# Kernel tuning notes

Measured on AMD Instinct MI355X. Metric: run time of the kernel, lower is better.

## Reference

```python
import jax, jax.numpy as jnp
import numpy as np

THRESH = 0.1          # affinity threshold from init_kwargs
SCALES = (1, 2, 4, 8, 16)  # dyadic diffusion scales 2^0..2^4


def compute_dist(X):
    # X: [N, d] -> squared-euclidean pairwise distances via Gram matrix
    G = X @ X.T
    dg = jnp.diag(G)
    return dg[None, :] + dg[:, None] - 2.0 * G


def _diffuse(P, F):
    # returns [P^1 F, P^2 F, P^4 F, P^8 F, P^16 F] via 16 sequential applies
    outs = []
    cur = F
    for step in range(1, SCALES[-1] + 1):
        cur = P @ cur
        if step in SCALES:
            outs.append(cur)
    return outs


def _wavelet_bank(P, F):
    # lazy diffusion wavelets: psi_0 = I - P, psi_j = P^{2^{j-1}} - P^{2^j}
    lows = [F] + _diffuse(P, F)            # t = 0,1,2,4,8,16
    psis = [lows[j] - lows[j + 1] for j in range(len(lows) - 1)]  # 5 wavelets
    return psis, lows[-1]                  # (wavelet coeffs, low-pass P^16 F)


def _gwt_features(X):
    # X: [N, d] reweighted point cloud -> [N, 16*d] scattering features
    N, d = X.shape
    W = jnp.exp(-compute_dist(X) / 10.0)
    W = jnp.where(W < THRESH, jnp.zeros_like(W), W)   # sparsify affinity
    deg = W.sum(axis=1, keepdims=True)                # self-loop w=1 => deg>=1
    P = 0.5 * (jnp.eye(N, dtype=X.dtype) + W / deg)   # lazy random walk
    psis, low = _wavelet_bank(P, X)
    firsts = [jnp.abs(p) for p in psis]
    U = jnp.concatenate(firsts, axis=1)               # [N, 5*d] diffuse all at once
    psis2, _ = _wavelet_bank(P, U)
    # second order: |psi_{j2} |psi_{j1} x|| only for j2 > j1 (10 pairs)
    seconds = [jnp.abs(psis2[j2][:, : j2 * d]) for j2 in range(1, len(psis2))]
    return jnp.concatenate([low] + firsts + seconds, axis=1)  # [N, (1+5+10)*d]


def setup_inputs() -> dict:
    key = jax.random.key(0)
    k1, k2 = jax.random.split(key)
    point_clouds = jax.random.normal(k1, (4, 2048, 3), dtype=jnp.float32)
    alphas = jax.random.uniform(k2, (4, 3), dtype=jnp.float32)  # learned param
    return {"point_clouds": point_clouds, "alphas": alphas}


def reference(point_clouds, alphas):
    # point_clouds: [B, N, d]; alphas: [K, d]
    Xb = point_clouds[:, None, :, :] * alphas[None, :, None, :]  # [B, K, N, d]
    feats = jax.vmap(jax.vmap(_gwt_features))(Xb)                # [B, K, N, 16d]
    # per-cloud: cat over K along feature dim then mean over nodes == mean then flatten
    return feats.mean(axis=2).reshape(feats.shape[0], -1)        # [B, K*16*d]
```

## Files before the change

### kernel.cpp

```cpp
#include <hip/hip_runtime.h>
#include <hip/hip_bf16.h>


#define NN 2048
#define NPAIR 16

typedef _Float16 half8 __attribute__((ext_vector_type(8)));
typedef _Float16 f16x2 __attribute__((ext_vector_type(2)));
typedef float f32x4 __attribute__((ext_vector_type(4)));

extern "C" __device__ f16x2 __ocml_exp2_2f16(f16x2);

#define C2F 0.28853900817779268f
#define CWF -0.14426950408889634f
#define NL2T 3.3219280948873623f

__global__ __launch_bounds__(256) void initpack_k(const float* __restrict__ pc,
                                                  const float* __restrict__ alphas,
                                                  float* __restrict__ Xs,
                                                  _Float16* __restrict__ XT,
                                                  _Float16* __restrict__ Xp) {
    int gid = blockIdx.x * 256 + threadIdx.x;
    if (gid >= NPAIR * NN) return;
    int p = gid >> 11, i = gid & (NN - 1);
    int b = p >> 2, k = p & 3;
    const float* pcr = pc + ((size_t)b * NN + i) * 3;
    const float* al  = alphas + k * 3;
    float x = pcr[0] * al[0], y = pcr[1] * al[1], z = pcr[2] * al[2];
    float q = CWF * (x * x + y * y + z * z);
    float4 o; o.x = x; o.y = y; o.z = z; o.w = q;
    ((float4*)Xs)[gid] = o;
    _Float16* xt = XT + (size_t)p * 16 * NN + i;
    xt[0 * NN] = (_Float16)x;
    xt[1 * NN] = (_Float16)y;
    xt[2 * NN] = (_Float16)z;
    xt[3 * NN] = (_Float16)1.0f;
#pragma unroll
    for (int n = 4; n < 16; ++n) xt[n * NN] = (_Float16)0.f;
    _Float16* xp = Xp + ((size_t)p * 1024 + (i >> 1)) * 8 + (i & 1);
    xp[0] = (_Float16)x; xp[2] = (_Float16)y;
    xp[4] = (_Float16)z; xp[6] = (_Float16)q;
}

template<bool FIRST, bool DUAL, bool BUILDU>
__global__ __launch_bounds__(512, DUAL ? 4 : 8)
void apply_k(const float* __restrict__ Xs, const _Float16* __restrict__ Xp,
             float* __restrict__ ihd,
             const _Float16* __restrict__ cur1, _Float16* __restrict__ out1,
             float* __restrict__ lvl1, int t1,
             const _Float16* __restrict__ cur2, _Float16* __restrict__ out2,
             float* __restrict__ lvl2, int t2,
             const float* __restrict__ LT1u, _Float16* __restrict__ UTp) {
    constexpr int SMSZ = DUAL ? 8192 : 4352;
    __shared__ __align__(16) float smem[SMSZ];
    const int tid  = threadIdx.x;
    const int lane = tid & 63;
    const int wv   = tid >> 6;
    const int p    = blockIdx.y;
    const int m0   = blockIdx.x * 32;
    const int idx16 = lane & 15, quad = lane >> 4;

    {
        const float4* src = (const float4*)(Xp + (size_t)p * 8192);
        float4* dst = (float4*)smem;
        dst[tid]       = src[tid];
        dst[tid + 512] = src[tid + 512];
    }
    __syncthreads();

    f16x2 qi2[2], xx2[2], xy2[2], xz2[2];
#pragma unroll
    for (int s = 0; s < 2; ++s) {
        float4 v = *(const float4*)(Xs + ((size_t)p * NN + m0 + s * 16 + idx16) * 4);
        _Float16 q = (_Float16)(v.w + NL2T);
        _Float16 x = (_Float16)(C2F * v.x);
        _Float16 y = (_Float16)(C2F * v.y);
        _Float16 z = (_Float16)(C2F * v.z);
        qi2[s] = (f16x2){q, q}; xx2[s] = (f16x2){x, x};
        xy2[s] = (f16x2){y, y}; xz2[s] = (f16x2){z, z};
    }
    const f16x2 SC2 = (f16x2){(_Float16)32768.f, (_Float16)32768.f};

    const _Float16* bp1 = cur1 + ((size_t)p * 16 + idx16) * NN + wv * 256 + quad * 8;
    const _Float16* bp2 = DUAL ? cur2 + ((size_t)p * 16 + idx16) * NN + wv * 256 + quad * 8
                               : nullptr;
    f32x4 acc1[2] = {{0.f,0.f,0.f,0.f},{0.f,0.f,0.f,0.f}};
    f32x4 acc2[2] = {{0.f,0.f,0.f,0.f},{0.f,0.f,0.f,0.f}};

    for (int kc = 0; kc < 8; ++kc) {
        const int pb = wv * 128 + kc * 16 + quad * 4;
        half8 bf1 = *(const half8*)(bp1 + kc * 32);
        half8 bf2;
        if (DUAL) bf2 = *(const half8*)(bp2 + kc * 32);
        union { f16x2 h2[4]; half8 h8; } af[2];
#pragma unroll
        for (int jp = 0; jp < 4; ++jp) {
            union { float4 f; f16x2 h[4]; } e;
            e.f = ((const float4*)smem)[pb + jp];
#pragma unroll
            for (int s = 0; s < 2; ++s) {
                f16x2 tv = qi2[s] + e.h[3];
                tv = __builtin_elementwise_fma(xx2[s], e.h[0], tv);
                tv = __builtin_elementwise_fma(xy2[s], e.h[1], tv);
                tv = __builtin_elementwise_fma(xz2[s], e.h[2], tv);
                f16x2 u = __builtin_elementwise_min(tv, tv * SC2);
                af[s].h2[jp] = __ocml_exp2_2f16(u);
            }
        }
#pragma unroll
        for (int s = 0; s < 2; ++s) {
            acc1[s] = __builtin_amdgcn_mfma_f32_16x16x32_f16(af[s].h8, bf1, acc1[s], 0, 0, 0);
            if (DUAL)
                acc2[s] = __builtin_amdgcn_mfma_f32_16x16x32_f16(af[s].h8, bf2, acc2[s], 0, 0, 0);
        }
    }

    const int n = tid & 15, rloc = tid >> 4;
    const int s2 = rloc >> 4, mloc = rloc & 15;
    const int base = s2 * 256 + (mloc >> 2) * 64 + (mloc & 3);
    const int row = m0 + rloc;
    float ihEff;
    if (!FIRST) ihEff = 0.1f * ihd[p * NN + row];

    __syncthreads();
#pragma unroll
    for (int s = 0; s < 2; ++s)
        *(f32x4*)&smem[wv * 512 + s * 256 + lane * 4] = acc1[s];
    if (DUAL) {
#pragma unroll
        for (int s = 0; s < 2; ++s)
            *(f32x4*)&smem[4096 + wv * 512 + s * 256 + lane * 4] = acc2[s];
    }
    __syncthreads();

    float o1v;
    {
        float sum = 0.f;
#pragma unroll
        for (int g = 0; g < 8; ++g) sum += smem[g * 512 + base + n * 4];
        if (FIRST) {
            float deg10 = 0.f;
#pragma unroll
            for (int g = 0; g < 8; ++g) deg10 += smem[g * 512 + base + 12];
            float ih = 5.0f / deg10;
            if (n == 3) ihd[p * NN + row] = ih;
            ihEff = 0.1f * ih;
        }
        float cv = (float)cur1[((size_t)p * 16 + n) * NN + row];
        o1v = 0.5f * cv + ihEff * sum;
        out1[((size_t)p * 16 + n) * NN + row] = (_Float16)o1v;
        if (lvl1) lvl1[(((size_t)p * 5 + t1) * 16 + n) * NN + row] = o1v;
    }
    if (DUAL) {
        float sum = 0.f;
#pragma unroll
        for (int g = 0; g < 8; ++g) sum += smem[4096 + g * 512 + base + n * 4];
        float cv = (float)cur2[((size_t)p * 16 + n) * NN + row];
        float o = 0.5f * cv + ihEff * sum;
        out2[((size_t)p * 16 + n) * NN + row] = (_Float16)o;
        if (lvl2) lvl2[(((size_t)p * 5 + t2) * 16 + n) * NN + row] = o;
    }
    if (BUILDU) {
        if (n < 3) smem[4096 + n * 32 + rloc] = o1v;
        __syncthreads();
        _Float16 uv = (_Float16)0.f;
        if (n < 12) {
            const int jw = n / 3, c = n - 3 * jw;
            float a = (jw == 0) ? Xs[((size_t)p * NN + row) * 4 + c]
                                : LT1u[(((size_t)p * 5 + (jw - 1)) * 16 + c) * NN + row];
            float bb = (jw == 3) ? smem[4096 + c * 32 + rloc]
                                 : LT1u[(((size_t)p * 5 + jw) * 16 + c) * NN + row];
            uv = (_Float16)fabsf(a - bb);
        }
        UTp[((size_t)p * 16 + n) * NN + row] = uv;
    }
}

__global__ __launch_bounds__(64) void reduce_k(const float* __restrict__ Xs,
                                               const float* __restrict__ LT1,
                                               const float* __restrict__ LT2,
                                               float* __restrict__ out) {
    int f = blockIdx.x, p = blockIdx.y, lane = threadIdx.x;
    const float* l1 = LT1 + (size_t)p * 5 * 16 * NN;
    const float* l2 = LT2 + (size_t)p * 5 * 16 * NN;
    float s = 0.f;
    for (int m = lane; m < NN; m += 64) {
        float v;
        if (f < 3) {
            v = l1[((size_t)4 * 16 + f) * NN + m];
        } else if (f < 18) {
            int j = (f - 3) / 3, c = (f - 3) % 3;
            float a = (j == 0) ? Xs[((size_t)p * NN + m) * 4 + c]
                               : l1[((size_t)(j - 1) * 16 + c) * NN + m];
            float b = l1[((size_t)j * 16 + c) * NN + m];
            v = fabsf(a - b);
        } else {
            int gg = f - 18, j2, uc;
            if (gg < 3)       { j2 = 1; uc = gg; }
            else if (gg < 9)  { j2 = 2; uc = gg - 3; }
            else if (gg < 18) { j2 = 3; uc = gg - 9; }
            else              { j2 = 4; uc = gg - 18; }
            v = fabsf(l2[((size_t)(j2 - 1) * 16 + uc) * NN + m]
                    - l2[((size_t)j2 * 16 + uc) * NN + m]);
        }
        s += v;
    }
#pragma unroll
    for (int off = 32; off > 0; off >>= 1) s += __shfl_down(s, off, 64);
    if (lane == 0) out[p * 48 + f] = s * (1.0f / NN);
}

extern "C" void kernel_launch(void* const* d_in, const int* in_sizes, int n_in,
                              void* d_out, int out_size, void* d_ws, size_t ws_size,
                              hipStream_t stream) {
    const float* pc     = (const float*)d_in[0];
    const float* alphas = (const float*)d_in[1];
    float* outp = (float*)d_out;

    char* base = (char*)d_ws;
    size_t off = 0;
    auto carve = [&](size_t bytes) -> void* {
        void* r = base + off;
        off = (off + bytes + 255) & ~(size_t)255;
        return r;
    };
    float*     Xs  = (float*)carve((size_t)NPAIR * NN * 4 * sizeof(float));
    _Float16*  Xp  = (_Float16*)carve((size_t)NPAIR * 1024 * 8 * 2);
    float*     ihd = (float*)carve((size_t)NPAIR * NN * sizeof(float));
    _Float16*  XT  = (_Float16*)carve((size_t)NPAIR * 16 * NN * 2);
    _Float16*  UT  = (_Float16*)carve((size_t)NPAIR * 16 * NN * 2);
    _Float16*  pA  = (_Float16*)carve((size_t)NPAIR * 16 * NN * 2);
    _Float16*  pB  = (_Float16*)carve((size_t)NPAIR * 16 * NN * 2);
    _Float16*  pC  = (_Float16*)carve((size_t)NPAIR * 16 * NN * 2);
    _Float16*  pD  = (_Float16*)carve((size_t)NPAIR * 16 * NN * 2);
    float*     LT1 = (float*)carve((size_t)NPAIR * 5 * 16 * NN * sizeof(float));
    float*     LT2 = (float*)carve((size_t)NPAIR * 5 * 16 * NN * sizeof(float));

    dim3 gridA(NN / 32, NPAIR);

    initpack_k<<<dim3((NPAIR * NN) / 256), 256, 0, stream>>>(pc, alphas, Xs, XT, Xp);

    const _Float16* c1 = XT;
    int slot = 0;
    for (int step = 1; step <= 8; ++step) {
        _Float16* o1 = (c1 == pA) ? pB : pA;
        bool sv = (step & (step - 1)) == 0;
        float* lv = sv ? LT1 : nullptr;
        if (step == 1)
            apply_k<true, false, false><<<gridA, 512, 0, stream>>>(Xs, Xp, ihd,
                c1, o1, lv, slot, nullptr, nullptr, nullptr, 0, nullptr, nullptr);
        else if (step == 8)
            apply_k<false, false, true><<<gridA, 512, 0, stream>>>(Xs, Xp, ihd,
                c1, o1, lv, slot, nullptr, nullptr, nullptr, 0, LT1, UT);
        else
            apply_k<false, false, false><<<gridA, 512, 0, stream>>>(Xs, Xp, ihd,
                c1, o1, lv, slot, nullptr, nullptr, nullptr, 0, nullptr, nullptr);
        if (sv) ++slot;
        c1 = o1;
    }

    const _Float16* c2 = UT;
    int slot2 = 0;
    for (int i = 1; i <= 8; ++i) {
        _Float16* o1 = (c1 == pA) ? pB : pA;
        _Float16* o2 = (c2 == pC) ? pD : pC;
        float* lv1 = (i == 8) ? LT1 : nullptr;
        bool sv2 = (i & (i - 1)) == 0;
        float* lv2 = sv2 ? LT2 : nullptr;
        apply_k<false, true, false><<<gridA, 512, 0, stream>>>(Xs, Xp, ihd,
            c1, o1, lv1, 4, c2, o2, lv2, slot2, nullptr, nullptr);
        if (sv2) ++slot2;
        c1 = o1; c2 = o2;
    }

    for (int i = 9; i <= 16; ++i) {
        _Float16* o2 = (c2 == pC) ? pD : pC;
        float* lv2 = (i == 16) ? LT2 : nullptr;
        apply_k<false, false, false><<<gridA, 512, 0, stream>>>(Xs, Xp, ihd,
            c2, o2, lv2, 4, nullptr, nullptr, nullptr, 0, nullptr, nullptr);
        c2 = o2;
    }

    reduce_k<<<dim3(48, NPAIR), 64, 0, stream>>>(Xs, LT1, LT2, outp);
}
```

Before: 484.1 us.

## Pack first-order chain and U signals into one 16-column diffusion stream

Before, steps 9-16 of the first-order diffusion and steps 1-8 of the second-order diffusion ran as two separate 16-column right-hand sides in a dual-MFMA kernel. Now, at step 8, the x-chain (columns 0-3) and the 12 |psi| columns share one 16-column buffer, so a single-RHS kernel is used for all 16 later steps. The dual kernel and its extra buffers are removed, and the reduction reads P^16 x from the second level table. The launch count stays the same, but each later launch does half the MFMA and B-operand traffic, and the dual kernel's lower occupancy bound goes away.

```diff
diff --git a/kernel.cpp b/kernel.cpp
--- a/kernel.cpp
+++ b/kernel.cpp
@@ -42,17 +42,14 @@
     xp[4] = (_Float16)z; xp[6] = (_Float16)q;
 }
 
-template<bool FIRST, bool DUAL, bool BUILDU>
-__global__ __launch_bounds__(512, DUAL ? 4 : 8)
+template<bool FIRST, bool BUILDU>
+__global__ __launch_bounds__(512, 8)
 void apply_k(const float* __restrict__ Xs, const _Float16* __restrict__ Xp,
              float* __restrict__ ihd,
-             const _Float16* __restrict__ cur1, _Float16* __restrict__ out1,
-             float* __restrict__ lvl1, int t1,
-             const _Float16* __restrict__ cur2, _Float16* __restrict__ out2,
-             float* __restrict__ lvl2, int t2,
-             const float* __restrict__ LT1u, _Float16* __restrict__ UTp) {
-    constexpr int SMSZ = DUAL ? 8192 : 4352;
-    __shared__ __align__(16) float smem[SMSZ];
+             const _Float16* __restrict__ cur, _Float16* __restrict__ out,
+             float* __restrict__ lvl, int t,
+             const float* __restrict__ LT1u) {
+    __shared__ __align__(16) float smem[4352];
     const int tid  = threadIdx.x;
     const int lane = tid & 63;
     const int wv   = tid >> 6;
@@ -81,17 +78,12 @@
     }
     const f16x2 SC2 = (f16x2){(_Float16)32768.f, (_Float16)32768.f};
 
-    const _Float16* bp1 = cur1 + ((size_t)p * 16 + idx16) * NN + wv * 256 + quad * 8;
-    const _Float16* bp2 = DUAL ? cur2 + ((size_t)p * 16 + idx16) * NN + wv * 256 + quad * 8
-                               : nullptr;
-    f32x4 acc1[2] = {{0.f,0.f,0.f,0.f},{0.f,0.f,0.f,0.f}};
-    f32x4 acc2[2] = {{0.f,0.f,0.f,0.f},{0.f,0.f,0.f,0.f}};
+    const _Float16* bp = cur + ((size_t)p * 16 + idx16) * NN + wv * 256 + quad * 8;
+    f32x4 acc[2] = {{0.f,0.f,0.f,0.f},{0.f,0.f,0.f,0.f}};
 
     for (int kc = 0; kc < 8; ++kc) {
         const int pb = wv * 128 + kc * 16 + quad * 4;
-        half8 bf1 = *(const half8*)(bp1 + kc * 32);
-        half8 bf2;
-        if (DUAL) bf2 = *(const half8*)(bp2 + kc * 32);
+        half8 bf = *(const half8*)(bp + kc * 32);
         union { f16x2 h2[4]; half8 h8; } af[2];
 #pragma unroll
         for (int jp = 0; jp < 4; ++jp) {
@@ -108,71 +100,54 @@
             }
         }
 #pragma unroll
-        for (int s = 0; s < 2; ++s) {
-            acc1[s] = __builtin_amdgcn_mfma_f32_16x16x32_f16(af[s].h8, bf1, acc1[s], 0, 0, 0);
-            if (DUAL)
-                acc2[s] = __builtin_amdgcn_mfma_f32_16x16x32_f16(af[s].h8, bf2, acc2[s], 0, 0, 0);
-        }
-    }
-
-    const int n = tid & 15, rloc = tid >> 4;
-    const int s2 = rloc >> 4, mloc = rloc & 15;
+        for (int s = 0; s < 2; ++s)
+            acc[s] = __builtin_amdgcn_mfma_f32_16x16x32_f16(af[s].h8, bf, acc[s], 0, 0, 0);
+    }
+
+    const int n  = tid >> 5;
+    const int rr = tid & 31;
+    const int s2 = rr >> 4, mloc = rr & 15;
     const int base = s2 * 256 + (mloc >> 2) * 64 + (mloc & 3);
-    const int row = m0 + rloc;
+    const int row = m0 + rr;
     float ihEff;
     if (!FIRST) ihEff = 0.1f * ihd[p * NN + row];
 
     __syncthreads();
 #pragma unroll
     for (int s = 0; s < 2; ++s)
-        *(f32x4*)&smem[wv * 512 + s * 256 + lane * 4] = acc1[s];
-    if (DUAL) {
-#pragma unroll
-        for (int s = 0; s < 2; ++s)
-            *(f32x4*)&smem[4096 + wv * 512 + s * 256 + lane * 4] = acc2[s];
-    }
+        *(f32x4*)&smem[wv * 512 + s * 256 + lane * 4] = acc[s];
     __syncthreads();
 
-    float o1v;
-    {
-        float sum = 0.f;
-#pragma unroll
-        for (int g = 0; g < 8; ++g) sum += smem[g * 512 + base + n * 4];
-        if (FIRST) {
-            float deg10 = 0.f;
-#pragma unroll
-            for (int g = 0; g < 8; ++g) deg10 += smem[g * 512 + base + 12];
-            float ih = 5.0f / deg10;
-            if (n == 3) ihd[p * NN + row] = ih;
-            ihEff = 0.1f * ih;
-        }
-        float cv = (float)cur1[((size_t)p * 16 + n) * NN + row];
-        o1v = 0.5f * cv + ihEff * sum;
-        out1[((size_t)p * 16 + n) * NN + row] = (_Float16)o1v;
-        if (lvl1) lvl1[(((size_t)p * 5 + t1) * 16 + n) * NN + row] = o1v;
-    }
-    if (DUAL) {
-        float sum = 0.f;
-#pragma unroll
-        for (int g = 0; g < 8; ++g) sum += smem[4096 + g * 512 + base + n * 4];
-        float cv = (float)cur2[((size_t)p * 16 + n) * NN + row];
-        float o = 0.5f * cv + ihEff * sum;
-        out2[((size_t)p * 16 + n) * NN + row] = (_Float16)o;
-        if (lvl2) lvl2[(((size_t)p * 5 + t2) * 16 + n) * NN + row] = o;
-    }
-    if (BUILDU) {
-        if (n < 3) smem[4096 + n * 32 + rloc] = o1v;
+    float sum = 0.f;
+#pragma unroll
+    for (int g = 0; g < 8; ++g) sum += smem[g * 512 + base + n * 4];
+    if (FIRST) {
+        float deg10 = 0.f;
+#pragma unroll
+        for (int g = 0; g < 8; ++g) deg10 += smem[g * 512 + base + 12];
+        float ih = 5.0f / deg10;
+        if (n == 3) ihd[p * NN + row] = ih;
+        ihEff = 0.1f * ih;
+    }
+    float cv = (float)cur[((size_t)p * 16 + n) * NN + row];
+    float o1v = 0.5f * cv + ihEff * sum;
+    if (lvl) lvl[(((size_t)p * 5 + t) * 16 + n) * NN + row] = o1v;
+
+    if (!BUILDU) {
+        out[((size_t)p * 16 + n) * NN + row] = (_Float16)o1v;
+    } else {
+        if (n < 3) smem[4096 + n * 32 + rr] = o1v;
         __syncthreads();
-        _Float16 uv = (_Float16)0.f;
-        if (n < 12) {
-            const int jw = n / 3, c = n - 3 * jw;
+        float oval = o1v;
+        if (n >= 4) {
+            const int u = n - 4, jw = u / 3, c = u - 3 * jw;
             float a = (jw == 0) ? Xs[((size_t)p * NN + row) * 4 + c]
                                 : LT1u[(((size_t)p * 5 + (jw - 1)) * 16 + c) * NN + row];
-            float bb = (jw == 3) ? smem[4096 + c * 32 + rloc]
+            float bb = (jw == 3) ? smem[4096 + c * 32 + rr]
                                  : LT1u[(((size_t)p * 5 + jw) * 16 + c) * NN + row];
-            uv = (_Float16)fabsf(a - bb);
+            oval = fabsf(a - bb);
         }
-        UTp[((size_t)p * 16 + n) * NN + row] = uv;
+        out[((size_t)p * 16 + n) * NN + row] = (_Float16)oval;
     }
 }
 
@@ -187,12 +162,13 @@
     for (int m = lane; m < NN; m += 64) {
         float v;
         if (f < 3) {
-            v = l1[((size_t)4 * 16 + f) * NN + m];
+            v = l2[((size_t)3 * 16 + f) * NN + m];
         } else if (f < 18) {
             int j = (f - 3) / 3, c = (f - 3) % 3;
             float a = (j == 0) ? Xs[((size_t)p * NN + m) * 4 + c]
                                : l1[((size_t)(j - 1) * 16 + c) * NN + m];
-            float b = l1[((size_t)j * 16 + c) * NN + m];
+            float b = (j < 4) ? l1[((size_t)j * 16 + c) * NN + m]
+                              : l2[((size_t)3 * 16 + c) * NN + m];
             v = fabsf(a - b);
         } else {
             int gg = f - 18, j2, uc;
@@ -200,8 +176,8 @@
             else if (gg < 9)  { j2 = 2; uc = gg - 3; }
             else if (gg < 18) { j2 = 3; uc = gg - 9; }
             else              { j2 = 4; uc = gg - 18; }
-            v = fabsf(l2[((size_t)(j2 - 1) * 16 + uc) * NN + m]
-                    - l2[((size_t)j2 * 16 + uc) * NN + m]);
+            v = fabsf(l2[((size_t)(j2 - 1) * 16 + uc + 4) * NN + m]
+                    - l2[((size_t)j2 * 16 + uc + 4) * NN + m]);
         }
         s += v;
     }
@@ -228,11 +204,8 @@
     _Float16*  Xp  = (_Float16*)carve((size_t)NPAIR * 1024 * 8 * 2);
     float*     ihd = (float*)carve((size_t)NPAIR * NN * sizeof(float));
     _Float16*  XT  = (_Float16*)carve((size_t)NPAIR * 16 * NN * 2);
-    _Float16*  UT  = (_Float16*)carve((size_t)NPAIR * 16 * NN * 2);
     _Float16*  pA  = (_Float16*)carve((size_t)NPAIR * 16 * NN * 2);
     _Float16*  pB  = (_Float16*)carve((size_t)NPAIR * 16 * NN * 2);
-    _Float16*  pC  = (_Float16*)carve((size_t)NPAIR * 16 * NN * 2);
-    _Float16*  pD  = (_Float16*)carve((size_t)NPAIR * 16 * NN * 2);
     float*     LT1 = (float*)carve((size_t)NPAIR * 5 * 16 * NN * sizeof(float));
     float*     LT2 = (float*)carve((size_t)NPAIR * 5 * 16 * NN * sizeof(float));
 
@@ -247,38 +220,27 @@
         bool sv = (step & (step - 1)) == 0;
         float* lv = sv ? LT1 : nullptr;
         if (step == 1)
-            apply_k<true, false, false><<<gridA, 512, 0, stream>>>(Xs, Xp, ihd,
-                c1, o1, lv, slot, nullptr, nullptr, nullptr, 0, nullptr, nullptr);
+            apply_k<true, false><<<gridA, 512, 0, stream>>>(Xs, Xp, ihd,
+                c1, o1, lv, slot, nullptr);
         else if (step == 8)
-            apply_k<false, false, true><<<gridA, 512, 0, stream>>>(Xs, Xp, ihd,
-                c1, o1, lv, slot, nullptr, nullptr, nullptr, 0, LT1, UT);
+            apply_k<false, true><<<gridA, 512, 0, stream>>>(Xs, Xp, ihd,
+                c1, o1, lv, slot, LT1);
         else
-            apply_k<false, false, false><<<gridA, 512, 0, stream>>>(Xs, Xp, ihd,
-                c1, o1, lv, slot, nullptr, nullptr, nullptr, 0, nullptr, nullptr);
+            apply_k<false, false><<<gridA, 512, 0, stream>>>(Xs, Xp, ihd,
+                c1, o1, lv, slot, nullptr);
         if (sv) ++slot;
         c1 = o1;
     }
 
-    const _Float16* c2 = UT;
     int slot2 = 0;
-    for (int i = 1; i <= 8; ++i) {
+    for (int i = 1; i <= 16; ++i) {
         _Float16* o1 = (c1 == pA) ? pB : pA;
-        _Float16* o2 = (c2 == pC) ? pD : pC;
-        float* lv1 = (i == 8) ? LT1 : nullptr;
-        bool sv2 = (i & (i - 1)) == 0;
-        float* lv2 = sv2 ? LT2 : nullptr;
-        apply_k<false, true, false><<<gridA, 512, 0, stream>>>(Xs, Xp, ihd,
-            c1, o1, lv1, 4, c2, o2, lv2, slot2, nullptr, nullptr);
-        if (sv2) ++slot2;
-        c1 = o1; c2 = o2;
-    }
-
-    for (int i = 9; i <= 16; ++i) {
-        _Float16* o2 = (c2 == pC) ? pD : pC;
-        float* lv2 = (i == 16) ? LT2 : nullptr;
-        apply_k<false, false, false><<<gridA, 512, 0, stream>>>(Xs, Xp, ihd,
-            c2, o2, lv2, 4, nullptr, nullptr, nullptr, 0, nullptr, nullptr);
-        c2 = o2;
+        bool sv = (i & (i - 1)) == 0;
+        float* lv = sv ? LT2 : nullptr;
+        apply_k<false, false><<<gridA, 512, 0, stream>>>(Xs, Xp, ihd,
+            c1, o1, lv, slot2, nullptr);
+        if (sv) ++slot2;
+        c1 = o1;
     }
 
     reduce_k<<<dim3(48, NPAIR), 64, 0, stream>>>(Xs, LT1, LT2, outp);
```

Measured after the change: 434.8 us. -10.2%, faster.
